# Optimization experiments

Hardware: AMD Instinct MI355X
Metric: run time of the kernel (lower is better)

Reference implementation:

```python
import jax, jax.numpy as jnp
import numpy as np

DEPTH = 16          # levels in the complete binary tree
D_IN = 256
H = 256
K = 2               # n_children
N_NODES = 2 ** DEPTH - 1  # 65535, heap/level order: children of node p at level l are (2p, 2p+1) at level l+1


def setup_inputs() -> dict:
    key = jax.random.key(0)
    ks = jax.random.split(key, 14)
    s = 0.05
    emb = jax.random.normal(ks[0], (N_NODES, D_IN), dtype=jnp.float32)
    mk = lambda k, shape: (jax.random.normal(k, shape, dtype=jnp.float32) * s)
    return {
        "emb": emb,
        "W_i": mk(ks[1], (H, D_IN)), "b_i": mk(ks[2], (H,)), "U_i": mk(ks[3], (K, H, H)),
        "W_o": mk(ks[4], (H, D_IN)), "b_o": mk(ks[5], (H,)), "U_o": mk(ks[6], (K, H, H)),
        "W_u": mk(ks[7], (H, D_IN)), "b_u": mk(ks[8], (H,)), "U_u": mk(ks[9], (K, H, H)),
        "W_f": mk(ks[10], (H, D_IN)), "b_f": mk(ks[11], (H,)), "U_f": mk(ks[12], (K, H, H)),
    }


def _node_batch(x, ch_h, ch_c, W_i, b_i, U_i, W_o, b_o, U_o, W_u, b_u, U_u, W_f, b_f, U_f):
    # x: [n, D_IN]; ch_h, ch_c: [n, K, H]
    # Linear: x @ W.T + b (torch layout W=[out,in]); U_k h = h @ U[k].T
    def gate(W, b, U):
        return x @ W.T + b + jnp.einsum("nkh,kdh->nd", ch_h, U)
    i = jax.nn.sigmoid(gate(W_i, b_i, U_i))
    o = jax.nn.sigmoid(gate(W_o, b_o, U_o))
    u = jnp.tanh(gate(W_u, b_u, U_u))
    # per-child forget gates: f_k = sigmoid(W_f x + U_f[k] h_k)
    f = jax.nn.sigmoid((x @ W_f.T + b_f)[:, None, :] + jnp.einsum("nkh,kdh->nkd", ch_h, U_f))
    c = i * u + jnp.sum(f * ch_c, axis=1)
    h = o * jnp.tanh(c)
    return h, c


def reference(emb, W_i, b_i, U_i, W_o, b_o, U_o, W_u, b_u, U_u, W_f, b_f, U_f):
    params = (W_i, b_i, U_i, W_o, b_o, U_o, W_u, b_u, U_u, W_f, b_f, U_f)
    # leaves: level DEPTH-1, zero children (matches zero-padding in node_forward)
    n = 2 ** (DEPTH - 1)
    start = n - 1
    zeros = jnp.zeros((n, K, H), dtype=emb.dtype)
    h, c = _node_batch(emb[start:start + n], zeros, zeros, *params)
    # bottom-up over internal levels; children of position p are (2p, 2p+1) in level below
    for l in range(DEPTH - 2, -1, -1):
        n = 2 ** l
        start = n - 1
        ch_h = h.reshape(n, K, H)
        ch_c = c.reshape(n, K, H)
        h, c = _node_batch(emb[start:start + n], ch_h, ch_c, *params)
    return h[0], c[0]  # root (hidden, cell), each [H]
```

## Files before the change

### kernel.cpp

```cpp
#include <hip/hip_runtime.h>
#include <hip/hip_bf16.h>
#include <cstdint>
#include <cstddef>


typedef __attribute__((ext_vector_type(8))) __bf16 bf16x8;
typedef __attribute__((ext_vector_type(4))) float floatx4;

#define TB 64

__device__ __forceinline__ float sigf(float x) { return 1.0f / (1.0f + __expf(-x)); }

__device__ __forceinline__ void load_lds16(const void* g, void* l) {
    __builtin_amdgcn_global_load_lds(
        (const __attribute__((address_space(1))) unsigned int*)g,
        (__attribute__((address_space(3))) unsigned int*)l, 16, 0, 0);
}

__global__ void pack_weights(const float* __restrict__ Wi, const float* __restrict__ bi, const float* __restrict__ Ui,
                             const float* __restrict__ Wo, const float* __restrict__ bo, const float* __restrict__ Uo,
                             const float* __restrict__ Wu, const float* __restrict__ bu, const float* __restrict__ Uu,
                             const float* __restrict__ Wf, const float* __restrict__ bf, const float* __restrict__ Uf,
                             __hip_bfloat16* __restrict__ Wpack, float* __restrict__ biasv)
{
    int m = blockIdx.x;
    int d = blockIdx.y;
    int k = threadIdx.x;
    const float* tbl[12] = {Wi, Wo, Wu, Wf,
                            Ui, Uo, Uu, Uf,
                            Ui + 65536, Uo + 65536, Uu + 65536, Uf + 65536};
    Wpack[((size_t)m * 256 + d) * 256 + k] = __float2bfloat16(tbl[m][d * 256 + k]);
    if (m < 4 && k == 0) {
        const float* bt[4] = {bi, bo, bu, bf};
        biasv[m * 256 + d] = bt[m][d];
    }
}

__global__ void convert_f32_bf16(const float* __restrict__ in, __hip_bfloat16* __restrict__ out, int n4)
{
    int i = blockIdx.x * 256 + threadIdx.x;
    if (i >= n4) return;
    float4 v = ((const float4*)in)[i];
    __hip_bfloat16 tmp[4];
    tmp[0] = __float2bfloat16(v.x);
    tmp[1] = __float2bfloat16(v.y);
    tmp[2] = __float2bfloat16(v.z);
    tmp[3] = __float2bfloat16(v.w);
    *(ushort4*)(out + (size_t)i * 4) = *(const ushort4*)tmp;
}

__global__ __launch_bounds__(256) void gemm_zx(
    const __hip_bfloat16* __restrict__ embB,
    const __hip_bfloat16* __restrict__ Wpack,
    const float* __restrict__ biasv,
    float* __restrict__ preZ,
    int M)
{
    __shared__ __hip_bfloat16 sA[64 * 32];
    __shared__ __hip_bfloat16 sB[64 * 32];
    const int t = threadIdx.x;
    const int s = blockIdx.x >> 2;
    const int d0 = (blockIdx.x & 3) * 64;
    const int bm0 = blockIdx.y * 64;
    const int lane = t & 63, w = t >> 6, lrow = lane & 15, q = lane >> 4;

    floatx4 acc[4];
    #pragma unroll
    for (int mt = 0; mt < 4; ++mt) acc[mt] = (floatx4){0.f, 0.f, 0.f, 0.f};

    for (int kk = 0; kk < 8; ++kk) {
        const int k0 = kk * 32;
        {
            int r = t >> 2, kc = t & 3;
            load_lds16(embB + (size_t)(bm0 + r) * 256 + k0 + kc * 8, &sA[t * 8]);
            load_lds16(Wpack + (size_t)(s * 256 + d0 + r) * 256 + k0 + kc * 8, &sB[t * 8]);
        }
        __syncthreads();
        bf16x8 af[4];
        #pragma unroll
        for (int mt = 0; mt < 4; ++mt)
            af[mt] = *(const bf16x8*)&sA[(mt * 16 + lrow) * 32 + q * 8];
        bf16x8 bfr = *(const bf16x8*)&sB[(w * 16 + lrow) * 32 + q * 8];
        #pragma unroll
        for (int mt = 0; mt < 4; ++mt)
            acc[mt] = __builtin_amdgcn_mfma_f32_16x16x32_bf16(af[mt], bfr, acc[mt], 0, 0, 0);
        __syncthreads();
    }

    const int d = d0 + w * 16 + lrow;
    const float bv = biasv[s * 256 + d];
    #pragma unroll
    for (int mt = 0; mt < 4; ++mt)
        #pragma unroll
        for (int rr = 0; rr < 4; ++rr) {
            int m = bm0 + mt * 16 + q * 4 + rr;
            if (m < M) preZ[(size_t)m * 1024 + s * 256 + d] = acc[mt][rr] + bv;
        }
}

template<int NS, int NP>
__global__ __launch_bounds__(256) void fused_level3(
    const __hip_bfloat16* __restrict__ embX,
    const __hip_bfloat16* __restrict__ hprev,
    const float* __restrict__ cprev,
    const __hip_bfloat16* __restrict__ Wpack,
    const float* __restrict__ biasv,
    __hip_bfloat16* __restrict__ hout,
    float* __restrict__ cout,
    int M)
{
    __shared__ __hip_bfloat16 sA[64 * 64];
    __shared__ __hip_bfloat16 sB[NS * 64 * 64];
    const int t = threadIdx.x;
    const int dchunk = blockIdx.x;
    const int bm0 = blockIdx.y * 64;
    const int lane = t & 63;
    const int w = t >> 6;
    const int lrow = lane & 15;
    const int q = lane >> 4;

    floatx4 accS[3][4];
    floatx4 accF[NP][4];
    #pragma unroll
    for (int s = 0; s < 3; ++s)
        #pragma unroll
        for (int mt = 0; mt < 4; ++mt) accS[s][mt] = (floatx4){0.f, 0.f, 0.f, 0.f};
    #pragma unroll
    for (int p = 0; p < NP; ++p)
        #pragma unroll
        for (int mt = 0; mt < 4; ++mt) accF[p][mt] = (floatx4){0.f, 0.f, 0.f, 0.f};

    #pragma unroll
    for (int p = 0; p < NP; ++p) {
        const __hip_bfloat16* Abase = (p == 0) ? embX : hprev;
        const int astride = (p == 0) ? 256 : 512;
        const int aoff = (p == 0) ? 0 : (p - 1) * 256;
        for (int kk = 0; kk < 4; ++kk) {
            const int k0 = kk * 64;
            #pragma unroll
            for (int rep = 0; rep < 2; ++rep) {
                int C = rep * 256 + t;
                int r = C >> 3, c0 = C & 7;
                load_lds16(Abase + (size_t)(bm0 + r) * astride + aoff + k0 + (c0 ^ (r & 7)) * 8,
                           &sA[C * 8]);
            }
            #pragma unroll
            for (int rep = 0; rep < NS * 2; ++rep) {
                int C = rep * 256 + t;
                int s = C >> 9, r = (C >> 3) & 63, c0 = C & 7;
                load_lds16(Wpack + (size_t)((p * 4 + s) * 256 + dchunk * 64 + r) * 256
                                 + k0 + (c0 ^ (r & 7)) * 8,
                           &sB[C * 8]);
            }
            __syncthreads();

            bf16x8 af[2][4];
            #pragma unroll
            for (int ks = 0; ks < 2; ++ks)
                #pragma unroll
                for (int mt = 0; mt < 4; ++mt)
                    af[ks][mt] = *(const bf16x8*)&sA[(mt * 16 + lrow) * 64
                                                     + (((ks * 4 + q) ^ (lrow & 7)) * 8)];
            #pragma unroll
            for (int s = 0; s < NS; ++s) {
                #pragma unroll
                for (int ks = 0; ks < 2; ++ks) {
                    bf16x8 bfr = *(const bf16x8*)&sB[(s * 64 + w * 16 + lrow) * 64
                                                     + (((ks * 4 + q) ^ (lrow & 7)) * 8)];
                    if (s < 3) {
                        #pragma unroll
                        for (int mt = 0; mt < 4; ++mt)
                            accS[s][mt] = __builtin_amdgcn_mfma_f32_16x16x32_bf16(af[ks][mt], bfr, accS[s][mt], 0, 0, 0);
                    } else {
                        #pragma unroll
                        for (int mt = 0; mt < 4; ++mt)
                            accF[p][mt] = __builtin_amdgcn_mfma_f32_16x16x32_bf16(af[ks][mt], bfr, accF[p][mt], 0, 0, 0);
                    }
                }
            }
            __syncthreads();
        }
    }

    const int d = dchunk * 64 + w * 16 + lrow;
    const float bI = biasv[d];
    const float bO = biasv[256 + d];
    const float bU = biasv[512 + d];
    const float bF = (NS == 4) ? biasv[768 + d] : 0.0f;
    #pragma unroll
    for (int mt = 0; mt < 4; ++mt) {
        #pragma unroll
        for (int rr = 0; rr < 4; ++rr) {
            const int m = bm0 + mt * 16 + q * 4 + rr;
            if (m >= M) continue;
            float iv = sigf(accS[0][mt][rr] + bI);
            float ov = sigf(accS[1][mt][rr] + bO);
            float uv = tanhf(accS[2][mt][rr] + bU);
            float c;
            if (NS == 4) {
                float fx = accF[0][mt][rr];
                float fl = sigf(fx + accF[NP >= 2 ? 1 : 0][mt][rr] + bF);
                float fr = sigf(fx + accF[NP >= 3 ? 2 : 0][mt][rr] + bF);
                c = iv * uv + fl * cprev[(size_t)m * 512 + d]
                            + fr * cprev[(size_t)m * 512 + 256 + d];
            } else {
                c = iv * uv;
            }
            cout[(size_t)m * 256 + d] = c;
            hout[(size_t)m * 256 + d] = __float2bfloat16(ov * tanhf(c));
        }
    }
}

__global__ __launch_bounds__(256) void tail_levels(
    __hip_bfloat16* __restrict__ hbuf, float* __restrict__ cbuf,
    const __hip_bfloat16* __restrict__ Wpack,
    const float* __restrict__ preZ,
    unsigned* __restrict__ bar, float* __restrict__ out)
{
    __shared__ __hip_bfloat16 sB[8 * 16 * 256];
    const int bid = blockIdx.x;
    const int t = threadIdx.x;
    const int dt = bid & 15;
    const int g = bid >> 4;
    const int w = t >> 6, lane = t & 63, lrow = lane & 15, q = lane >> 4;

    for (int rnd = 0; rnd < 16; ++rnd) {
        int C = rnd * 256 + t;
        int q8k = C & 31, r = (C >> 5) & 15, m8 = C >> 9;
        load_lds16(Wpack + (size_t)((4 + m8) * 256 + dt * 16 + r) * 256 + (q8k ^ (r & 7)) * 8,
                   &sB[(size_t)C * 8]);
    }
    __syncthreads();

    const int d = dt * 16 + lrow;
    unsigned barnum = 0;
    unsigned snum = 0;

    for (int l = 10; l >= 0; --l) {
        if (l <= 6 && g != 0) break;

        const int n = 1 << l;
        const int start = n - 1;
        const int startc = 2 * n - 1;
        const __hip_bfloat16* hp = hbuf + (size_t)startc * 256;
        const float* cp = cbuf + (size_t)startc * 256;
        __hip_bfloat16* ho = hbuf + (size_t)start * 256;
        float* co = cbuf + (size_t)start * 256;
        const int nmt = (n + 15) >> 4;
        const int slot   = (l > 6) ? (g * 4 + w) : w;
        const int stride = (l > 6) ? 16 : 4;

        for (int mt = slot; mt < nmt; mt += stride) {
            const int m0 = mt * 16;
            bf16x8 af[2][8];
            #pragma unroll
            for (int p = 0; p < 2; ++p)
                #pragma unroll
                for (int kk = 0; kk < 8; ++kk)
                    af[p][kk] = *(const bf16x8*)(hp + (size_t)(m0 + lrow) * 512 + p * 256 + kk * 32 + q * 8);
            float zi[4][4], clr[2][4];
            #pragma unroll
            for (int rr = 0; rr < 4; ++rr) {
                int m = m0 + q * 4 + rr;
                #pragma unroll
                for (int s = 0; s < 4; ++s)
                    zi[s][rr] = preZ[(size_t)(start + m) * 1024 + s * 256 + d];
                clr[0][rr] = cp[(size_t)m * 512 + d];
                clr[1][rr] = cp[(size_t)m * 512 + 256 + d];
            }

            floatx4 accS[3], accF1, accF2;
            #pragma unroll
            for (int s = 0; s < 3; ++s)
                accS[s] = (floatx4){zi[s][0], zi[s][1], zi[s][2], zi[s][3]};
            accF1 = (floatx4){0.f, 0.f, 0.f, 0.f};
            accF2 = (floatx4){0.f, 0.f, 0.f, 0.f};

            #pragma unroll
            for (int p = 0; p < 2; ++p)
                #pragma unroll
                for (int kk = 0; kk < 8; ++kk)
                    #pragma unroll
                    for (int s = 0; s < 4; ++s) {
                        bf16x8 bfr = *(const bf16x8*)&sB[((p * 4 + s) * 16 + lrow) * 256
                                                         + (((kk * 4 + q) ^ (lrow & 7)) * 8)];
                        if (s < 3)
                            accS[s] = __builtin_amdgcn_mfma_f32_16x16x32_bf16(af[p][kk], bfr, accS[s], 0, 0, 0);
                        else if (p == 0)
                            accF1 = __builtin_amdgcn_mfma_f32_16x16x32_bf16(af[p][kk], bfr, accF1, 0, 0, 0);
                        else
                            accF2 = __builtin_amdgcn_mfma_f32_16x16x32_bf16(af[p][kk], bfr, accF2, 0, 0, 0);
                    }

            #pragma unroll
            for (int rr = 0; rr < 4; ++rr) {
                int m = m0 + q * 4 + rr;
                if (m >= n) continue;
                float iv = sigf(accS[0][rr]);
                float ov = sigf(accS[1][rr]);
                float uv = tanhf(accS[2][rr]);
                float fx = zi[3][rr];
                float fl = sigf(fx + accF1[rr]);
                float fr = sigf(fx + accF2[rr]);
                float c = iv * uv + fl * clr[0][rr] + fr * clr[1][rr];
                float hv = ov * tanhf(c);
                if (l == 0) {
                    out[d] = hv;
                    out[256 + d] = c;
                } else {
                    co[(size_t)m * 256 + d] = c;
                    ho[(size_t)m * 256 + d] = __float2bfloat16(hv);
                }
            }
        }

        if (l > 0) {
            __syncthreads();
            if (l > 6) {
                ++barnum;
                if (t == 0) {
                    unsigned v = __hip_atomic_fetch_add(&bar[0], 1, __ATOMIC_ACQ_REL,
                                                        __HIP_MEMORY_SCOPE_AGENT) + 1;
                    if (v == barnum * 64u) {
                        __hip_atomic_fetch_add(&bar[64], 1, __ATOMIC_RELEASE,
                                               __HIP_MEMORY_SCOPE_AGENT);
                    } else {
                        while (__hip_atomic_load(&bar[64], __ATOMIC_RELAXED,
                                                 __HIP_MEMORY_SCOPE_AGENT) < barnum)
                            __builtin_amdgcn_s_sleep(1);
                    }
                }
            } else {
                ++snum;
                if (t == 0) {
                    unsigned v = __hip_atomic_fetch_add(&bar[128], 1, __ATOMIC_ACQ_REL,
                                                        __HIP_MEMORY_SCOPE_AGENT) + 1;
                    if (v == snum * 16u) {
                        __hip_atomic_fetch_add(&bar[192], 1, __ATOMIC_RELEASE,
                                               __HIP_MEMORY_SCOPE_AGENT);
                    } else {
                        while (__hip_atomic_load(&bar[192], __ATOMIC_RELAXED,
                                                 __HIP_MEMORY_SCOPE_AGENT) < snum)
                            __builtin_amdgcn_s_sleep(1);
                    }
                }
            }
            __syncthreads();
            __builtin_amdgcn_fence(__ATOMIC_ACQUIRE, "agent");
        }
    }
}

extern "C" void kernel_launch(void* const* d_in, const int* in_sizes, int n_in,
                              void* d_out, int out_size, void* d_ws, size_t ws_size,
                              hipStream_t stream)
{
    const float* emb = (const float*)d_in[0];
    const float* Wi  = (const float*)d_in[1];
    const float* bi  = (const float*)d_in[2];
    const float* Ui  = (const float*)d_in[3];
    const float* Wo  = (const float*)d_in[4];
    const float* bo  = (const float*)d_in[5];
    const float* Uo  = (const float*)d_in[6];
    const float* Wu  = (const float*)d_in[7];
    const float* bu  = (const float*)d_in[8];
    const float* Uu  = (const float*)d_in[9];
    const float* Wf  = (const float*)d_in[10];
    const float* bf  = (const float*)d_in[11];
    const float* Uf  = (const float*)d_in[12];

    char* p = (char*)d_ws;
    __hip_bfloat16* Wpack = (__hip_bfloat16*)p;  p += (size_t)12 * 256 * 256 * 2;
    float* biasv          = (float*)p;           p += (size_t)4 * 256 * 4;
    __hip_bfloat16* embB  = (__hip_bfloat16*)p;  p += (size_t)65535 * 256 * 2;
    __hip_bfloat16* hbuf  = (__hip_bfloat16*)p;  p += (size_t)65535 * 256 * 2;
    float* cbuf           = (float*)p;           p += (size_t)65535 * 256 * 4;
    float* preZ           = (float*)p;           p += (size_t)2047 * 1024 * 4;
    unsigned* bar         = (unsigned*)p;        p += 1024;

    pack_weights<<<dim3(12, 256), 256, 0, stream>>>(Wi, bi, Ui, Wo, bo, Uo, Wu, bu, Uu, Wf, bf, Uf,
                                                    Wpack, biasv);
    convert_f32_bf16<<<(65535 * 256 / 4 + 255) / 256, 256, 0, stream>>>(emb, embB, 65535 * 256 / 4);

    gemm_zx<<<dim3(16, 32), 256, 0, stream>>>(embB, Wpack, biasv, preZ, 2047);

    {
        const int n = 32768, start = n - 1;
        fused_level3<3, 1><<<dim3(4, n / 64), 256, 0, stream>>>(
            embB + (size_t)start * 256, nullptr, nullptr, Wpack, biasv,
            hbuf + (size_t)start * 256, cbuf + (size_t)start * 256, n);
    }
    for (int l = 14; l >= 11; --l) {
        const int n = 1 << l;
        const int start = n - 1;
        const int startc = 2 * n - 1;
        fused_level3<4, 3><<<dim3(4, n / 64), 256, 0, stream>>>(
            embB + (size_t)start * 256,
            hbuf + (size_t)startc * 256,
            cbuf + (size_t)startc * 256,
            Wpack, biasv,
            hbuf + (size_t)start * 256, cbuf + (size_t)start * 256, n);
    }

    hipMemsetAsync(bar, 0, 1024, stream);
    tail_levels<<<TB, 256, 0, stream>>>(hbuf, cbuf, Wpack, preZ, bar, (float*)d_out);
}
```

Before: 399.2 us.

## Fuse fp32-to-bf16 embedding conversion into GEMM loads and use hierarchical grid barrier

Removes the standalone embedding conversion kernel and its bf16 buffer. The GEMM and level kernels now read fp32 embeddings and convert them in registers before storing to LDS, which avoids a full write and re-read of the embedding table. The grid barrier in the tail kernel becomes two-level, with 8 group counters feeding one global counter, to reduce atomic contention. The barrier memset moves to the start of the stream. In exchange, the direct global-to-LDS loads for the embedding tile become synchronous register loads.

New measurement: 420.5 us. +5.3%, slower.

```diff
diff --git a/kernel.cpp b/kernel.cpp
--- a/kernel.cpp
+++ b/kernel.cpp
@@ -15,6 +15,17 @@
     __builtin_amdgcn_global_load_lds(
         (const __attribute__((address_space(1))) unsigned int*)g,
         (__attribute__((address_space(3))) unsigned int*)l, 16, 0, 0);
+}
+
+__device__ __forceinline__ bf16x8 cvt8(const float* p) {
+    float4 v0 = *(const float4*)p;
+    float4 v1 = *(const float4*)(p + 4);
+    __hip_bfloat16 tmp[8];
+    tmp[0] = __float2bfloat16(v0.x); tmp[1] = __float2bfloat16(v0.y);
+    tmp[2] = __float2bfloat16(v0.z); tmp[3] = __float2bfloat16(v0.w);
+    tmp[4] = __float2bfloat16(v1.x); tmp[5] = __float2bfloat16(v1.y);
+    tmp[6] = __float2bfloat16(v1.z); tmp[7] = __float2bfloat16(v1.w);
+    return *(const bf16x8*)tmp;
 }
 
 __global__ void pack_weights(const float* __restrict__ Wi, const float* __restrict__ bi, const float* __restrict__ Ui,
@@ -36,21 +47,8 @@
     }
 }
 
-__global__ void convert_f32_bf16(const float* __restrict__ in, __hip_bfloat16* __restrict__ out, int n4)
-{
-    int i = blockIdx.x * 256 + threadIdx.x;
-    if (i >= n4) return;
-    float4 v = ((const float4*)in)[i];
-    __hip_bfloat16 tmp[4];
-    tmp[0] = __float2bfloat16(v.x);
-    tmp[1] = __float2bfloat16(v.y);
-    tmp[2] = __float2bfloat16(v.z);
-    tmp[3] = __float2bfloat16(v.w);
-    *(ushort4*)(out + (size_t)i * 4) = *(const ushort4*)tmp;
-}
-
 __global__ __launch_bounds__(256) void gemm_zx(
-    const __hip_bfloat16* __restrict__ embB,
+    const float* __restrict__ emb,
     const __hip_bfloat16* __restrict__ Wpack,
     const float* __restrict__ biasv,
     float* __restrict__ preZ,
@@ -72,7 +70,7 @@
         const int k0 = kk * 32;
         {
             int r = t >> 2, kc = t & 3;
-            load_lds16(embB + (size_t)(bm0 + r) * 256 + k0 + kc * 8, &sA[t * 8]);
+            *(bf16x8*)&sA[t * 8] = cvt8(emb + (size_t)(bm0 + r) * 256 + k0 + kc * 8);
             load_lds16(Wpack + (size_t)(s * 256 + d0 + r) * 256 + k0 + kc * 8, &sB[t * 8]);
         }
         __syncthreads();
@@ -100,7 +98,7 @@
 
 template<int NS, int NP>
 __global__ __launch_bounds__(256) void fused_level3(
-    const __hip_bfloat16* __restrict__ embX,
+    const float* __restrict__ embX,
     const __hip_bfloat16* __restrict__ hprev,
     const float* __restrict__ cprev,
     const __hip_bfloat16* __restrict__ Wpack,
@@ -132,17 +130,25 @@
 
     #pragma unroll
     for (int p = 0; p < NP; ++p) {
-        const __hip_bfloat16* Abase = (p == 0) ? embX : hprev;
-        const int astride = (p == 0) ? 256 : 512;
-        const int aoff = (p == 0) ? 0 : (p - 1) * 256;
         for (int kk = 0; kk < 4; ++kk) {
             const int k0 = kk * 64;
-            #pragma unroll
-            for (int rep = 0; rep < 2; ++rep) {
-                int C = rep * 256 + t;
-                int r = C >> 3, c0 = C & 7;
-                load_lds16(Abase + (size_t)(bm0 + r) * astride + aoff + k0 + (c0 ^ (r & 7)) * 8,
-                           &sA[C * 8]);
+            if (p == 0) {
+                #pragma unroll
+                for (int rep = 0; rep < 2; ++rep) {
+                    int C = rep * 256 + t;
+                    int r = C >> 3, c0 = C & 7;
+                    *(bf16x8*)&sA[C * 8] =
+                        cvt8(embX + (size_t)(bm0 + r) * 256 + k0 + (c0 ^ (r & 7)) * 8);
+                }
+            } else {
+                #pragma unroll
+                for (int rep = 0; rep < 2; ++rep) {
+                    int C = rep * 256 + t;
+                    int r = C >> 3, c0 = C & 7;
+                    load_lds16(hprev + (size_t)(bm0 + r) * 512 + (p - 1) * 256
+                                     + k0 + (c0 ^ (r & 7)) * 8,
+                               &sA[C * 8]);
+                }
             }
             #pragma unroll
             for (int rep = 0; rep < NS * 2; ++rep) {
@@ -320,27 +326,34 @@
             if (l > 6) {
                 ++barnum;
                 if (t == 0) {
-                    unsigned v = __hip_atomic_fetch_add(&bar[0], 1, __ATOMIC_ACQ_REL,
+                    const int grp = bid & 7;
+                    unsigned v = __hip_atomic_fetch_add(&bar[grp * 16], 1, __ATOMIC_ACQ_REL,
                                                         __HIP_MEMORY_SCOPE_AGENT) + 1;
-                    if (v == barnum * 64u) {
-                        __hip_atomic_fetch_add(&bar[64], 1, __ATOMIC_RELEASE,
-                                               __HIP_MEMORY_SCOPE_AGENT);
-                    } else {
-                        while (__hip_atomic_load(&bar[64], __ATOMIC_RELAXED,
+                    bool released = false;
+                    if (v == barnum * 8u) {
+                        unsigned gv = __hip_atomic_fetch_add(&bar[128], 1, __ATOMIC_ACQ_REL,
+                                                             __HIP_MEMORY_SCOPE_AGENT) + 1;
+                        if (gv == barnum * 8u) {
+                            __hip_atomic_fetch_add(&bar[144], 1, __ATOMIC_RELEASE,
+                                                   __HIP_MEMORY_SCOPE_AGENT);
+                            released = true;
+                        }
+                    }
+                    if (!released)
+                        while (__hip_atomic_load(&bar[144], __ATOMIC_RELAXED,
                                                  __HIP_MEMORY_SCOPE_AGENT) < barnum)
                             __builtin_amdgcn_s_sleep(1);
-                    }
                 }
             } else {
                 ++snum;
                 if (t == 0) {
-                    unsigned v = __hip_atomic_fetch_add(&bar[128], 1, __ATOMIC_ACQ_REL,
+                    unsigned v = __hip_atomic_fetch_add(&bar[160], 1, __ATOMIC_ACQ_REL,
                                                         __HIP_MEMORY_SCOPE_AGENT) + 1;
                     if (v == snum * 16u) {
-                        __hip_atomic_fetch_add(&bar[192], 1, __ATOMIC_RELEASE,
+                        __hip_atomic_fetch_add(&bar[176], 1, __ATOMIC_RELEASE,
                                                __HIP_MEMORY_SCOPE_AGENT);
                     } else {
-                        while (__hip_atomic_load(&bar[192], __ATOMIC_RELAXED,
+                        while (__hip_atomic_load(&bar[176], __ATOMIC_RELAXED,
                                                  __HIP_MEMORY_SCOPE_AGENT) < snum)
                             __builtin_amdgcn_s_sleep(1);
                     }
@@ -373,22 +386,21 @@
     char* p = (char*)d_ws;
     __hip_bfloat16* Wpack = (__hip_bfloat16*)p;  p += (size_t)12 * 256 * 256 * 2;
     float* biasv          = (float*)p;           p += (size_t)4 * 256 * 4;
-    __hip_bfloat16* embB  = (__hip_bfloat16*)p;  p += (size_t)65535 * 256 * 2;
     __hip_bfloat16* hbuf  = (__hip_bfloat16*)p;  p += (size_t)65535 * 256 * 2;
     float* cbuf           = (float*)p;           p += (size_t)65535 * 256 * 4;
     float* preZ           = (float*)p;           p += (size_t)2047 * 1024 * 4;
     unsigned* bar         = (unsigned*)p;        p += 1024;
 
+    hipMemsetAsync(bar, 0, 1024, stream);
     pack_weights<<<dim3(12, 256), 256, 0, stream>>>(Wi, bi, Ui, Wo, bo, Uo, Wu, bu, Uu, Wf, bf, Uf,
                                                     Wpack, biasv);
-    convert_f32_bf16<<<(65535 * 256 / 4 + 255) / 256, 256, 0, stream>>>(emb, embB, 65535 * 256 / 4);
-
-    gemm_zx<<<dim3(16, 32), 256, 0, stream>>>(embB, Wpack, biasv, preZ, 2047);
+
+    gemm_zx<<<dim3(16, 32), 256, 0, stream>>>(emb, Wpack, biasv, preZ, 2047);
 
     {
         const int n = 32768, start = n - 1;
         fused_level3<3, 1><<<dim3(4, n / 64), 256, 0, stream>>>(
-            embB + (size_t)start * 256, nullptr, nullptr, Wpack, biasv,
+            emb + (size_t)start * 256, nullptr, nullptr, Wpack, biasv,
             hbuf + (size_t)start * 256, cbuf + (size_t)start * 256, n);
     }
     for (int l = 14; l >= 11; --l) {
@@ -396,13 +408,12 @@
         const int start = n - 1;
         const int startc = 2 * n - 1;
         fused_level3<4, 3><<<dim3(4, n / 64), 256, 0, stream>>>(
-            embB + (size_t)start * 256,
+            emb + (size_t)start * 256,
             hbuf + (size_t)startc * 256,
             cbuf + (size_t)startc * 256,
             Wpack, biasv,
             hbuf + (size_t)start * 256, cbuf + (size_t)start * 256, n);
     }
 
-    hipMemsetAsync(bar, 0, 1024, stream);
     tail_levels<<<TB, 256, 0, stream>>>(hbuf, cbuf, Wpack, preZ, bar, (float*)d_out);
 }
```
